# Performance work log

Hardware: AMD Instinct MI355X
Metric: run time of the kernel (lower is better)

Reference implementation:

```python
import jax, jax.numpy as jnp
import numpy as np

N_QUBITS = 20
N_TERMS = 4
BATCH = 16
DIM = 2 ** N_QUBITS


def _apply_two_qubit_gate(state, U, q0, q1):
    """Apply batched 4x4 unitary U (B,4,4) to qubit axes (q0,q1) of state (2,)*n+(B,)."""
    s = jnp.moveaxis(state, (q0, q1), (0, 1))
    rest = s.shape[2:-1]
    B = s.shape[-1]
    s = s.reshape(4, -1, B)  # (4, rest, B)
    out = jnp.einsum('bij,jrb->irb', U, s)
    out = out.reshape((2, 2) + rest + (B,))
    return jnp.moveaxis(out, (0, 1), (q0, q1))


def setup_inputs() -> dict:
    key = jax.random.key(0)
    k1, k2, k3, k4, k5 = jax.random.split(key, 5)
    H_real = jax.random.normal(k1, (N_TERMS, 4, 4), jnp.float32)
    H_imag = jax.random.normal(k2, (N_TERMS, 4, 4), jnp.float32)
    tevo = jax.random.uniform(k3, (N_TERMS, BATCH), jnp.float32)
    state_real = jax.random.normal(k4, (DIM, BATCH), jnp.float32)
    state_imag = jax.random.normal(k5, (DIM, BATCH), jnp.float32)
    nrm = jnp.sqrt(jnp.sum(state_real ** 2 + state_imag ** 2, axis=0, keepdims=True))
    return {'H_real': H_real, 'H_imag': H_imag, 'tevo': tevo,
            'state_real': state_real / nrm, 'state_imag': state_imag / nrm}


def reference(H_real, H_imag, tevo, state_real, state_imag):
    # Hermitian generators per term: H_k = (A + A^H)/2, A = H_real + i*H_imag  -> (K,4,4)
    A = H_real + 1j * H_imag
    H = 0.5 * (A + jnp.conj(jnp.swapaxes(A, -1, -2)))
    # Hamiltonian evolution U_k(t) = exp(-i H_k t) via eigendecomposition (HEvoPyQOperation)
    w, V = jnp.linalg.eigh(H)                       # w: (K,4) real, V: (K,4,4)
    phases = jnp.exp(-1j * w[:, None, :] * tevo[:, :, None])  # (K,B,4)
    U = jnp.einsum('kij,kbj,klj->kbil', V, phases, jnp.conj(V))  # (K,B,4,4)
    # statevector (2,)*n + (B,)
    state = (state_real + 1j * state_imag).reshape((2,) * N_QUBITS + (BATCH,))
    # AddPyQOperation: reduce(add, (op(state, values) for op in operations))
    out = jnp.zeros_like(state)
    for k in range(N_TERMS):
        out = out + _apply_two_qubit_gate(state, U[k], k, k + 1)
    out = out.reshape(DIM, BATCH)
    return jnp.stack([jnp.real(out), jnp.imag(out)])  # (2, DIM, B) real view of complex output
```

## Files before the change

kernel.cpp:

```cpp
#include <hip/hip_runtime.h>

#define NQ 20
#define DIMQ (1 << NQ)
#define NB 16
#define NT 4
#define RBITS 15
#define NCOL (1 << (RBITS + 4))

#define USTRIDE 36
#define UTOT (64 * USTRIDE)

__device__ __forceinline__ void cfma(float2& o, const float2 u, const float2 s) {
  asm("v_pk_fma_f32 %0, %1, %2, %0 op_sel_hi:[0,1,1]\n\t"
      "v_pk_fma_f32 %0, %1, %2, %0 op_sel:[1,1,0] op_sel_hi:[1,0,1] neg_lo:[1,0,0]"
      : "+v"(o) : "v"(u), "v"(s));
}
__device__ __forceinline__ float2 cmul(const float2 u, const float2 s) {
  float2 o;
  asm("v_pk_mul_f32 %0, %1, %2 op_sel_hi:[0,1]\n\t"
      "v_pk_fma_f32 %0, %1, %2, %0 op_sel:[1,1,0] op_sel_hi:[1,0,1] neg_lo:[1,0,0]"
      : "=&v"(o) : "v"(u), "v"(s));
  return o;
}

__global__ __launch_bounds__(256) void compute_u_kernel(
    const float* __restrict__ Hre, const float* __restrict__ Him,
    const float* __restrict__ tevo, float* __restrict__ uout) {
  __shared__ float er_s[64][4][4];
  __shared__ float ei_s[64][4][4];

  const int tid  = threadIdx.x;
  const int task = tid >> 2;
  const int row  = tid & 3;
  const int k    = task >> 4;
  const int b    = task & 15;

  float Ar[4][4], Ai[4][4];
#pragma unroll
  for (int i = 0; i < 4; i++) {
#pragma unroll
    for (int j = 0; j < 4; j++) {
      Ar[i][j] = Hre[k * 16 + i * 4 + j];
      Ai[i][j] = Him[k * 16 + i * 4 + j];
    }
  }
  const float t = tevo[k * NB + b];
  const float ts = t * (1.0f / 16.0f);

  float Gr[4][4], Gi[4][4];
#pragma unroll
  for (int i = 0; i < 4; i++) {
#pragma unroll
    for (int j = 0; j < 4; j++) {
      const float hr = 0.5f * (Ar[i][j] + Ar[j][i]);
      const float hi = 0.5f * (Ai[i][j] - Ai[j][i]);
      Gr[i][j] = ts * hi;
      Gi[i][j] = -ts * hr;
    }
  }

  float Er[4], Ei[4], Tr[4], Ti[4];
#pragma unroll
  for (int j = 0; j < 4; j++) {
    Er[j] = (j == row) ? 1.0f : 0.0f;
    Ei[j] = 0.0f;
    Tr[j] = Er[j];
    Ti[j] = 0.0f;
  }
#pragma unroll
  for (int m = 1; m <= 8; m++) {
    const float inv = 1.0f / (float)m;
    float nr[4], ni[4];
#pragma unroll
    for (int j = 0; j < 4; j++) {
      float ar = 0.0f, ai = 0.0f;
#pragma unroll
      for (int p = 0; p < 4; p++) {
        ar += Tr[p] * Gr[p][j] - Ti[p] * Gi[p][j];
        ai += Tr[p] * Gi[p][j] + Ti[p] * Gr[p][j];
      }
      nr[j] = ar * inv;
      ni[j] = ai * inv;
    }
#pragma unroll
    for (int j = 0; j < 4; j++) {
      Tr[j] = nr[j]; Ti[j] = ni[j];
      Er[j] += nr[j]; Ei[j] += ni[j];
    }
  }

  for (int q = 0; q < 4; q++) {
    __syncthreads();
#pragma unroll
    for (int j = 0; j < 4; j++) {
      er_s[task][row][j] = Er[j];
      ei_s[task][row][j] = Ei[j];
    }
    __syncthreads();
    float nr[4], ni[4];
#pragma unroll
    for (int j = 0; j < 4; j++) {
      float ar = 0.0f, ai = 0.0f;
#pragma unroll
      for (int p = 0; p < 4; p++) {
        ar += Er[p] * er_s[task][p][j] - Ei[p] * ei_s[task][p][j];
        ai += Er[p] * ei_s[task][p][j] + Ei[p] * er_s[task][p][j];
      }
      nr[j] = ar; ni[j] = ai;
    }
#pragma unroll
    for (int j = 0; j < 4; j++) { Er[j] = nr[j]; Ei[j] = ni[j]; }
  }

  const int ubase = (k * 16 + b) * USTRIDE;
#pragma unroll
  for (int j = 0; j < 4; j++) {
    uout[ubase + (row * 4 + j) * 2]     = Er[j];
    uout[ubase + (row * 4 + j) * 2 + 1] = Ei[j];
  }
}

__global__ __launch_bounds__(256, 4) void apply_gates_kernel(
    const float* __restrict__ sre, const float* __restrict__ sim,
    const float* __restrict__ u, float* __restrict__ out) {
  __shared__ __align__(16) float ul[UTOT];
  __shared__ __align__(16) float st[32 * 128];
  const int tid = threadIdx.x;
  const int w   = tid >> 6;
  const int l   = tid & 63;
  const int c0  = blockIdx.x * 64;
  const int b   = l & 15;
  const int q0  = w & 1;

#pragma unroll
  for (int t = 0; t < 4; t++) {
    const int p   = w * 4 + t;
    const int sub = l >> 4;
    const int g   = 2 * p + (sub >> 1);
    const float* base = (sub & 1) ? sim : sre;
    const float* src  = base + (g << 19) + c0 + (l & 15) * 4;
    float* dst = st + p * 256;
    __builtin_amdgcn_global_load_lds(
        (const __attribute__((address_space(1))) float*)(const void*)src,
        (__attribute__((address_space(3))) float*)(void*)dst, 16, 0, 0);
  }

#pragma unroll
  for (int q = 0; q < 9; q++) ul[tid + q * 256] = u[tid + q * 256];

  __syncthreads();

  float2 s[8];
#pragma unroll
  for (int m = 0; m < 8; m++) {
    const int a = (w * 8 + m) * 128 + l;
    s[m].x = st[a];
    s[m].y = st[a + 64];
  }

  float2 o[8];

  {
    const float* ub = &ul[(3 * 16 + b) * USTRIDE];
#pragma unroll
    for (int i = 0; i < 4; i++) {
      const float4 v0 = *(const float4*)(ub + i * 8);
      const float4 v1 = *(const float4*)(ub + i * 8 + 4);
      const float2 u0 = make_float2(v0.x, v0.y), u1 = make_float2(v0.z, v0.w);
      const float2 u2 = make_float2(v1.x, v1.y), u3 = make_float2(v1.z, v1.w);
#pragma unroll
      for (int h = 0; h < 2; h++) {
        const int om = h * 4 + i;
        o[om] = cmul(u0, s[h * 4 + 0]);
        cfma(o[om], u1, s[h * 4 + 1]);
        cfma(o[om], u2, s[h * 4 + 2]);
        cfma(o[om], u3, s[h * 4 + 3]);
      }
    }
  }

  {
    const float* ub = &ul[(2 * 16 + b) * USTRIDE];
#pragma unroll
    for (int i = 0; i < 4; i++) {
      const float4 v0 = *(const float4*)(ub + i * 8);
      const float4 v1 = *(const float4*)(ub + i * 8 + 4);
      const float2 u0 = make_float2(v0.x, v0.y), u1 = make_float2(v0.z, v0.w);
      const float2 u2 = make_float2(v1.x, v1.y), u3 = make_float2(v1.z, v1.w);
#pragma unroll
      for (int l0 = 0; l0 < 2; l0++) {
        const int om = i * 2 + l0;
        cfma(o[om], u0, s[l0]);
        cfma(o[om], u1, s[2 + l0]);
        cfma(o[om], u2, s[4 + l0]);
        cfma(o[om], u3, s[6 + l0]);
      }
    }
  }

  {
    float2 p[8];
    const int pq = w ^ 1;
#pragma unroll
    for (int m = 0; m < 8; m++) {
      const int a = (pq * 8 + m) * 128 + l;
      p[m].x = st[a];
      p[m].y = st[a + 64];
    }
    const float* ub1 = &ul[(1 * 16 + b) * USTRIDE];
#pragma unroll
    for (int mh = 0; mh < 2; mh++) {
      const int i = q0 * 2 + mh;
      const float* row = ub1 + i * 8;
#pragma unroll
      for (int j2 = 0; j2 < 2; j2++) {
        const float2 uo = *(const float2*)(row + (q0 * 2 + j2) * 2);
        const float2 up = *(const float2*)(row + ((q0 ^ 1) * 2 + j2) * 2);
#pragma unroll
        for (int ml = 0; ml < 4; ml++) {
          const int om = mh * 4 + ml;
          cfma(o[om], uo, s[j2 * 4 + ml]);
          cfma(o[om], up, p[j2 * 4 + ml]);
        }
      }
    }
    const float* ub0 = &ul[b * USTRIDE];
    const float2 u01 = *(const float2*)(ub0 + (w * 4 + (w ^ 1)) * 2);
#pragma unroll
    for (int m = 0; m < 8; m++) cfma(o[m], u01, p[m]);
  }

  {
    const float* ub0 = &ul[b * USTRIDE];
    const float2 u00 = *(const float2*)(ub0 + (w * 4 + w) * 2);
#pragma unroll
    for (int m = 0; m < 8; m++) cfma(o[m], u00, s[m]);
#pragma unroll
    for (int d = 2; d < 4; d++) {
      const int jq = w ^ d;
      const float2 uj = *(const float2*)(ub0 + (w * 4 + jq) * 2);
#pragma unroll
      for (int m = 0; m < 8; m++) {
        const int a = (jq * 8 + m) * 128 + l;
        float2 t;
        t.x = st[a];
        t.y = st[a + 64];
        cfma(o[m], uj, t);
      }
    }
  }

#pragma unroll
  for (int m = 0; m < 8; m++) {
    const int off = c0 + l + ((w * 8 + m) << 19);
    __builtin_nontemporal_store(o[m].x, out + off);
    __builtin_nontemporal_store(o[m].y, out + off + (1 << 24));
  }
}

extern "C" void kernel_launch(void* const* d_in, const int* in_sizes, int n_in,
                              void* d_out, int out_size, void* d_ws, size_t ws_size,
                              hipStream_t stream) {
  const float* Hre  = (const float*)d_in[0];
  const float* Him  = (const float*)d_in[1];
  const float* tevo = (const float*)d_in[2];
  const float* sre  = (const float*)d_in[3];
  const float* sim  = (const float*)d_in[4];
  float* out = (float*)d_out;
  float* uws = (float*)d_ws;

  compute_u_kernel<<<1, 256, 0, stream>>>(Hre, Him, tevo, uws);
  apply_gates_kernel<<<NCOL / 64, 256, 0, stream>>>(sre, sim, uws, out);
}
```

Measured before the change: 50.45 us.

## Process four column tiles per block with double-buffered LDS prefetch

Each block now handles four consecutive 64-column tiles instead of one, so the grid is four times smaller. While one tile is computed, the next tile's state is prefetched into a second LDS buffer with async global-to-LDS loads, using a vmcnt wait and a barrier between tiles. This spreads the per-block unitary staging over more work and overlaps loads with compute and stores. The cost is twice the state LDS per block, which may lower occupancy, plus an extra barrier on each tile.

```diff
diff --git a/kernel.cpp b/kernel.cpp
--- a/kernel.cpp
+++ b/kernel.cpp
@@ -6,6 +6,8 @@
 #define NT 4
 #define RBITS 15
 #define NCOL (1 << (RBITS + 4))
+#define TILES 4
+#define NBLK (NCOL / 64 / TILES)
 
 #define USTRIDE 36
 #define UTOT (64 * USTRIDE)
@@ -120,18 +122,9 @@
   }
 }
 
-__global__ __launch_bounds__(256, 4) void apply_gates_kernel(
-    const float* __restrict__ sre, const float* __restrict__ sim,
-    const float* __restrict__ u, float* __restrict__ out) {
-  __shared__ __align__(16) float ul[UTOT];
-  __shared__ __align__(16) float st[32 * 128];
-  const int tid = threadIdx.x;
-  const int w   = tid >> 6;
-  const int l   = tid & 63;
-  const int c0  = blockIdx.x * 64;
-  const int b   = l & 15;
-  const int q0  = w & 1;
-
+__device__ __forceinline__ void dma_tile(const float* __restrict__ sre,
+                                         const float* __restrict__ sim,
+                                         int c0, float* dst_base, int w, int l) {
 #pragma unroll
   for (int t = 0; t < 4; t++) {
     const int p   = w * 4 + t;
@@ -139,17 +132,17 @@
     const int g   = 2 * p + (sub >> 1);
     const float* base = (sub & 1) ? sim : sre;
     const float* src  = base + (g << 19) + c0 + (l & 15) * 4;
-    float* dst = st + p * 256;
+    float* dst = dst_base + p * 256;
     __builtin_amdgcn_global_load_lds(
         (const __attribute__((address_space(1))) float*)(const void*)src,
         (__attribute__((address_space(3))) float*)(void*)dst, 16, 0, 0);
   }
-
-#pragma unroll
-  for (int q = 0; q < 9; q++) ul[tid + q * 256] = u[tid + q * 256];
-
-  __syncthreads();
-
+}
+
+__device__ __forceinline__ void compute_tile(const float* __restrict__ st,
+                                             const float* __restrict__ ul,
+                                             int c0, int w, int l, int b, int q0,
+                                             float* __restrict__ out) {
   float2 s[8];
 #pragma unroll
   for (int m = 0; m < 8; m++) {
@@ -255,6 +248,37 @@
     const int off = c0 + l + ((w * 8 + m) << 19);
     __builtin_nontemporal_store(o[m].x, out + off);
     __builtin_nontemporal_store(o[m].y, out + off + (1 << 24));
+  }
+}
+
+__global__ __launch_bounds__(256, 4) void apply_gates_kernel(
+    const float* __restrict__ sre, const float* __restrict__ sim,
+    const float* __restrict__ u, float* __restrict__ out) {
+  __shared__ __align__(16) float ul[UTOT];
+  __shared__ __align__(16) float st[2][32 * 128];
+  const int tid = threadIdx.x;
+  const int w   = tid >> 6;
+  const int l   = tid & 63;
+  const int b   = l & 15;
+  const int q0  = w & 1;
+  const int tbase = blockIdx.x * TILES;
+
+  dma_tile(sre, sim, tbase * 64, st[0], w, l);
+#pragma unroll
+  for (int q = 0; q < 9; q++) ul[tid + q * 256] = u[tid + q * 256];
+  __syncthreads();
+
+#pragma unroll
+  for (int t = 0; t < TILES; t++) {
+    if (t + 1 < TILES)
+      dma_tile(sre, sim, (tbase + t + 1) * 64, st[(t + 1) & 1], w, l);
+
+    compute_tile(st[t & 1], ul, (tbase + t) * 64, w, l, b, q0, out);
+
+    if (t + 1 < TILES) {
+      asm volatile("s_waitcnt vmcnt(16)" ::: "memory");
+      __builtin_amdgcn_s_barrier();
+    }
   }
 }
 
@@ -270,5 +294,5 @@
   float* uws = (float*)d_ws;
 
   compute_u_kernel<<<1, 256, 0, stream>>>(Hre, Him, tevo, uws);
-  apply_gates_kernel<<<NCOL / 64, 256, 0, stream>>>(sre, sim, uws, out);
-}
+  apply_gates_kernel<<<NBLK, 256, 0, stream>>>(sre, sim, uws, out);
+}
```

After: 75.50 us. 1.5x slower.
